# Kernel optimization log

Measured on AMD Instinct MI355X. Metric: run time of the kernel, lower is better.

## Reference

```python
import jax, jax.numpy as jnp
import numpy as np

N = 50000      # nodes
E = 800000     # edges (before self-loops)
DIN = 384
D = 128        # hidden_dim == output_dim
H = 4          # heads
FH = D // H    # per-head dim
B = 64         # graphs in batch
NEG = 0.2      # LeakyReLU slope in GATConv
EPS = 1e-5     # LayerNorm eps


def setup_inputs() -> dict:
    key = jax.random.key(0)
    ks = jax.random.split(key, 24)
    s = 0.02
    inp = {
        'node_features': jax.random.normal(ks[0], (N, DIN), jnp.float32),
        'edge_index': jax.random.randint(ks[1], (2, E), 0, N, dtype=jnp.int64),
        'edge_weight': jax.random.uniform(ks[2], (E,), jnp.float32),
        'batch': jnp.sort(jax.random.randint(ks[3], (N,), 0, B, dtype=jnp.int64)),
        # input projection
        'Wp': jax.random.normal(ks[4], (DIN, D), jnp.float32) * s,
        'bp': jnp.zeros((D,), jnp.float32),
    }
    for l in range(2):
        o = 5 + l * 9
        inp[f'W{l}'] = jax.random.normal(ks[o], (D, D), jnp.float32) * s      # lin_src (shared src/dst)
        inp[f'as{l}'] = jax.random.normal(ks[o + 1], (H, FH), jnp.float32) * s  # att_src
        inp[f'ad{l}'] = jax.random.normal(ks[o + 2], (H, FH), jnp.float32) * s  # att_dst
        inp[f'We{l}'] = jax.random.normal(ks[o + 3], (D,), jnp.float32) * s   # lin_edge (edge_dim=1)
        inp[f'ae{l}'] = jax.random.normal(ks[o + 4], (H, FH), jnp.float32) * s  # att_edge
        inp[f'b{l}'] = jnp.zeros((D,), jnp.float32)                           # GATConv bias
        inp[f'g{l}'] = jnp.ones((D,), jnp.float32)                            # LayerNorm gamma
        inp[f'be{l}'] = jnp.zeros((D,), jnp.float32)                          # LayerNorm beta
    return inp


def _gat(x, src, dst, ew, W, a_s, a_d, We, a_e, b):
    """PyG GATConv(in, D/H, heads=H, edge_dim=1), eval mode. ew includes self-loops."""
    n = x.shape[0]
    h = (x @ W).reshape(n, H, FH)                      # [N,H,FH]
    a_src = jnp.einsum('nhf,hf->nh', h, a_s)           # [N,H]
    a_dst = jnp.einsum('nhf,hf->nh', h, a_d)
    e = (ew[:, None] * We[None, :]).reshape(-1, H, FH)  # edge_dim=1 linear, no bias
    a_eg = jnp.einsum('ehf,hf->eh', e, a_e)            # [E,H]
    alpha = jax.nn.leaky_relu(a_src[src] + a_dst[dst] + a_eg, NEG)
    # softmax over incoming edges of each dst node
    amax = jax.ops.segment_max(alpha, dst, num_segments=n)
    amax = jnp.where(jnp.isfinite(amax), amax, 0.0)
    ex = jnp.exp(alpha - amax[dst])
    denom = jax.ops.segment_sum(ex, dst, num_segments=n)
    coef = ex / (denom[dst] + 1e-16)                   # [E,H]
    msg = h[src] * coef[..., None]                     # [E,H,FH]
    out = jax.ops.segment_sum(msg, dst, num_segments=n).reshape(n, D)
    return out + b


def _ln(x, g, b):
    mu = x.mean(-1, keepdims=True)
    v = ((x - mu) ** 2).mean(-1, keepdims=True)
    return (x - mu) * jax.lax.rsqrt(v + EPS) * g + b


def reference(node_features, edge_index, edge_weight, batch, Wp, bp,
              W0, as0, ad0, We0, ae0, b0, g0, be0,
              W1, as1, ad1, We1, ae1, b1, g1, be1):
    n = node_features.shape[0]
    # PyG GATConv add_self_loops=True, fill_value='mean' for edge_attr
    loop = jnp.arange(n, dtype=edge_index.dtype)
    src = jnp.concatenate([edge_index[0], loop])
    dst = jnp.concatenate([edge_index[1], loop])
    ew = jnp.concatenate([edge_weight, jnp.full((n,), edge_weight.mean(), edge_weight.dtype)])

    x = node_features @ Wp + bp
    for (W, a_s, a_d, We, a_e, b, g, be) in (
        (W0, as0, ad0, We0, ae0, b0, g0, be0),
        (W1, as1, ad1, We1, ae1, b1, g1, be1),
    ):
        res = x
        y = _gat(x, src, dst, ew, W, a_s, a_d, We, a_e, b)
        y = jax.nn.elu(_ln(y, g, be))
        x = y + res  # shapes match (hidden == output)

    # global_mean_pool
    s = jax.ops.segment_sum(x, batch, num_segments=B)
    c = jax.ops.segment_sum(jnp.ones((n,), x.dtype), batch, num_segments=B)
    return s / jnp.maximum(c, 1.0)[:, None]
```

## Files before the change

### kernel.cpp

```cpp
#include <hip/hip_runtime.h>

#define N_NODES 50000
#define N_EDGES 800000
#define DIN 384
#define DH 128
#define NB 64
#define NEG 0.2f

__device__ __forceinline__ float bf2f(unsigned short u) {
    return __uint_as_float((unsigned)u << 16);
}
__device__ __forceinline__ unsigned short f2bf(float x) {
    unsigned u = __float_as_uint(x);
    return (unsigned short)((u + 0x7fff + ((u >> 16) & 1)) >> 16);
}
__device__ __forceinline__ float sel4(float4 v, int k) {
    float r = v.x;
    r = (k == 1) ? v.y : r;
    r = (k == 2) ? v.z : r;
    r = (k == 3) ? v.w : r;
    return r;
}
using us8 = __attribute__((ext_vector_type(8))) unsigned short;

__global__ __launch_bounds__(256) void histew_kernel(const int* __restrict__ dst,
                                                     const float* __restrict__ ew,
                                                     int* __restrict__ cnt,
                                                     int* __restrict__ rank,
                                                     float* __restrict__ ews) {
    __shared__ float sred[4];
    const int tid = threadIdx.x;
    float v = 0.0f;
    for (int i = blockIdx.x * 256 + tid; i < N_EDGES; i += gridDim.x * 256) {
        rank[i] = atomicAdd(&cnt[dst[i]], 1);
        v += ew[i];
    }
    #pragma unroll
    for (int o = 32; o; o >>= 1) v += __shfl_down(v, o, 64);
    if ((tid & 63) == 0) sred[tid >> 6] = v;
    __syncthreads();
    if (tid == 0) atomicAdd(ews, sred[0] + sred[1] + sred[2] + sred[3]);
}

__global__ void scan_a(const int* __restrict__ cnt, int* __restrict__ scanned,
                       int* __restrict__ bsums) {
    __shared__ int s[256];
    int tid = threadIdx.x;
    int i = blockIdx.x * 256 + tid;
    int v = (i < N_NODES) ? cnt[i] : 0;
    s[tid] = v; __syncthreads();
    for (int o = 1; o < 256; o <<= 1) {
        int t = (tid >= o) ? s[tid - o] : 0;
        __syncthreads();
        s[tid] += t;
        __syncthreads();
    }
    if (i < N_NODES) scanned[i] = s[tid] - v;
    if (tid == 255) bsums[blockIdx.x] = s[255];
}

__global__ void scan_b(int* __restrict__ bsums, int nb,
                       const float* __restrict__ We0, const float* __restrict__ ae0,
                       const float* __restrict__ We1, const float* __restrict__ ae1,
                       const float* __restrict__ ews, float* __restrict__ consts) {
    __shared__ int s[256];
    int tid = threadIdx.x;
    int v = (tid < nb) ? bsums[tid] : 0;
    s[tid] = v; __syncthreads();
    for (int o = 1; o < 256; o <<= 1) {
        int t = (tid >= o) ? s[tid - o] : 0;
        __syncthreads();
        s[tid] += t;
        __syncthreads();
    }
    if (tid < nb) bsums[tid] = s[tid] - v;

    if (tid < 64) {
        const int l = tid;
        float p00 = We0[l] * ae0[l];
        float p01 = We0[l + 64] * ae0[l + 64];
        float p10 = We1[l] * ae1[l];
        float p11 = We1[l + 64] * ae1[l + 64];
        #pragma unroll
        for (int o = 1; o < 32; o <<= 1) {
            p00 += __shfl_xor(p00, o, 64); p01 += __shfl_xor(p01, o, 64);
            p10 += __shfl_xor(p10, o, 64); p11 += __shfl_xor(p11, o, 64);
        }
        const float c0 = __shfl(p00, 0, 64), c1 = __shfl(p00, 32, 64);
        const float c2 = __shfl(p01, 0, 64), c3 = __shfl(p01, 32, 64);
        const float d0 = __shfl(p10, 0, 64), d1 = __shfl(p10, 32, 64);
        const float d2 = __shfl(p11, 0, 64), d3 = __shfl(p11, 32, 64);
        if (l == 0) {
            consts[0] = c0; consts[1] = c1; consts[2] = c2; consts[3] = c3;
            consts[4] = d0; consts[5] = d1; consts[6] = d2; consts[7] = d3;
            consts[8] = ews[0] * (1.0f / N_EDGES);
        }
    }
}

__global__ void scan_c(const int* __restrict__ scanned, const int* __restrict__ bsums,
                       const int* __restrict__ cnt, int* __restrict__ ptr) {
    int i = blockIdx.x * 256 + threadIdx.x;
    if (i < N_NODES) {
        int p = scanned[i] + bsums[blockIdx.x];
        ptr[i] = p;
        if (i == N_NODES - 1) ptr[N_NODES] = p + cnt[i];
    }
}

__global__ __launch_bounds__(256) void fill_kernel(const int* __restrict__ src,
                            const int* __restrict__ dst,
                            const float* __restrict__ ew,
                            const int* __restrict__ rank,
                            const int* __restrict__ ptr,
                            int2* __restrict__ recE) {
    const int e0 = (blockIdx.x * 256 + threadIdx.x) * 4;
    if (e0 >= N_EDGES) return;
    const int4 d4 = *(const int4*)(dst + e0);
    const int4 s4 = *(const int4*)(src + e0);
    const int4 r4 = *(const int4*)(rank + e0);
    const float4 w4 = *(const float4*)(ew + e0);
    recE[ptr[d4.x] + r4.x] = make_int2(s4.x, __float_as_int(w4.x));
    recE[ptr[d4.y] + r4.y] = make_int2(s4.y, __float_as_int(w4.y));
    recE[ptr[d4.z] + r4.z] = make_int2(s4.z, __float_as_int(w4.z));
    recE[ptr[d4.w] + r4.w] = make_int2(s4.w, __float_as_int(w4.w));
}

template<int K, bool BF16OUT>
__global__ __launch_bounds__(256) void mfma_gemm(const float* __restrict__ A,
                                                 const float* __restrict__ W,
                                                 const float* __restrict__ bias,
                                                 void* __restrict__ Cv, int M,
                                                 const float* __restrict__ a_s,
                                                 const float* __restrict__ a_d,
                                                 float* __restrict__ asrc_o,
                                                 float* __restrict__ adst_o)
{
    constexpr int BM = 64, BK = 32;
    constexpr int LS = 40;
    __shared__ unsigned short As[BM * LS];
    __shared__ unsigned short Bs[DH * LS];
    using short8 = __attribute__((ext_vector_type(8))) short;
    using f32x4  = __attribute__((ext_vector_type(4))) float;

    const int tid = threadIdx.x;
    const int w = tid >> 6, l = tid & 63;
    const int lane16 = l & 15, quad = l >> 4;
    const int m0 = blockIdx.x * BM;

    f32x4 acc[8] = {};

    const int ar = tid >> 2, af = tid & 3;
    int arow = m0 + ar; if (arow >= M) arow = M - 1;
    const float* Ap = A + (size_t)arow * K;
    const int bn = tid & 127, bq = tid >> 7;

    for (int k0 = 0; k0 < K; k0 += BK) {
        __syncthreads();
        #pragma unroll
        for (int i = 0; i < 2; ++i) {
            const int f4 = af + 4 * i;
            float4 v = *(const float4*)(Ap + k0 + f4 * 4);
            ushort4 u = {f2bf(v.x), f2bf(v.y), f2bf(v.z), f2bf(v.w)};
            *(ushort4*)&As[ar * LS + f4 * 4] = u;
        }
        #pragma unroll
        for (int i = 0; i < 4; ++i) {
            const int kq = bq + 2 * i;
            float v0 = W[(size_t)(k0 + kq * 4 + 0) * DH + bn];
            float v1 = W[(size_t)(k0 + kq * 4 + 1) * DH + bn];
            float v2 = W[(size_t)(k0 + kq * 4 + 2) * DH + bn];
            float v3 = W[(size_t)(k0 + kq * 4 + 3) * DH + bn];
            ushort4 u = {f2bf(v0), f2bf(v1), f2bf(v2), f2bf(v3)};
            *(ushort4*)&Bs[bn * LS + kq * 4] = u;
        }
        __syncthreads();
        short8 afrag = *(short8*)&As[(w * 16 + lane16) * LS + quad * 8];
        #pragma unroll
        for (int nt = 0; nt < 8; ++nt) {
            short8 bfrag = *(short8*)&Bs[(nt * 16 + lane16) * LS + quad * 8];
            acc[nt] = __builtin_amdgcn_mfma_f32_16x16x32_bf16(afrag, bfrag, acc[nt], 0, 0, 0);
        }
    }

    const int orow0 = m0 + w * 16 + quad * 4;
    #pragma unroll
    for (int nt = 0; nt < 8; ++nt) {
        const int col = nt * 16 + lane16;
        const float bv = BF16OUT ? 0.0f : bias[col];
        #pragma unroll
        for (int r = 0; r < 4; ++r) {
            const int row = orow0 + r;
            if (row < M) {
                if constexpr (BF16OUT)
                    ((unsigned short*)Cv)[(size_t)row * DH + col] = f2bf(acc[nt][r]);
                else
                    ((float*)Cv)[(size_t)row * DH + col] = acc[nt][r] + bv;
            }
        }
    }

    if constexpr (BF16OUT) {
        float psh[4][4] = {}, pdh[4][4] = {};
        #pragma unroll
        for (int nt = 0; nt < 8; ++nt) {
            const int hd = nt >> 1;
            const float asv = a_s[nt * 16 + lane16];
            const float adv = a_d[nt * 16 + lane16];
            #pragma unroll
            for (int r = 0; r < 4; ++r) {
                psh[hd][r] = fmaf(acc[nt][r], asv, psh[hd][r]);
                pdh[hd][r] = fmaf(acc[nt][r], adv, pdh[hd][r]);
            }
        }
        #pragma unroll
        for (int o = 1; o < 16; o <<= 1) {
            #pragma unroll
            for (int hd = 0; hd < 4; ++hd)
                #pragma unroll
                for (int r = 0; r < 4; ++r) {
                    psh[hd][r] += __shfl_xor(psh[hd][r], o, 64);
                    pdh[hd][r] += __shfl_xor(pdh[hd][r], o, 64);
                }
        }
        if (lane16 == 0) {
            #pragma unroll
            for (int r = 0; r < 4; ++r) {
                const int row = orow0 + r;
                if (row < M) {
                    float4 o1 = {psh[0][r], psh[1][r], psh[2][r], psh[3][r]};
                    float4 o2 = {pdh[0][r], pdh[1][r], pdh[2][r], pdh[3][r]};
                    *(float4*)(asrc_o + (size_t)row * 4) = o1;
                    *(float4*)(adst_o + (size_t)row * 4) = o2;
                }
            }
        }
    }
}

#define MSG_NPB 16
__global__ __launch_bounds__(256) void msg_kernel(
    const unsigned short* __restrict__ h, const float* __restrict__ asrc,
    const float* __restrict__ adst, const float* __restrict__ xres,
    const int* __restrict__ indptr, const int2* __restrict__ recE,
    const float* __restrict__ consts, const int layer,
    const float* __restrict__ bias, const float* __restrict__ gamma,
    const float* __restrict__ beta, float* __restrict__ xout)
{
    const int l = threadIdx.x & 63;
    const int wv = threadIdx.x >> 6;
    const int grp = l >> 4;
    const int c8 = l & 15;
    const int hd8 = c8 >> 2;

    const int n = blockIdx.x * MSG_NPB + wv * 4 + grp;

    const float4 ccv = *(const float4*)(consts + layer * 4);
    const float cc_l = sel4(ccv, hd8);
    const float ewm = consts[8];
    const unsigned short* hb = h + c8 * 8;

    const int st = indptr[n];
    const int deg = indptr[n + 1] - st;
    const float ad_l = adst[(size_t)n * 4 + hd8];
    const float as_l = asrc[(size_t)n * 4 + hd8];

    float a0 = as_l + ad_l + ewm * cc_l;
    a0 = a0 > 0.f ? a0 : NEG * a0;
    const float pv0_l = __expf(a0);

    float dsum = 0.f;
    float acc8[8];
    {
        us8 u = *(const us8*)(hb + (size_t)n * DH);
        #pragma unroll
        for (int i = 0; i < 8; ++i) acc8[i] = pv0_l * bf2f(u[i]);
    }

    const int2* rq = recE + st;
    int e = 0;
    for (; e + 3 < deg; e += 4) {
        const int2 r0 = rq[e],     r1 = rq[e + 1];
        const int2 r2 = rq[e + 2], r3 = rq[e + 3];
        const float av0 = asrc[(size_t)r0.x * 4 + hd8];
        const float av1 = asrc[(size_t)r1.x * 4 + hd8];
        const float av2 = asrc[(size_t)r2.x * 4 + hd8];
        const float av3 = asrc[(size_t)r3.x * 4 + hd8];
        us8 u0 = *(const us8*)(hb + (size_t)r0.x * DH);
        us8 u1 = *(const us8*)(hb + (size_t)r1.x * DH);
        us8 u2 = *(const us8*)(hb + (size_t)r2.x * DH);
        us8 u3 = *(const us8*)(hb + (size_t)r3.x * DH);
        float al0 = av0 + ad_l + __int_as_float(r0.y) * cc_l;
        float al1 = av1 + ad_l + __int_as_float(r1.y) * cc_l;
        float al2 = av2 + ad_l + __int_as_float(r2.y) * cc_l;
        float al3 = av3 + ad_l + __int_as_float(r3.y) * cc_l;
        al0 = al0 > 0.f ? al0 : NEG * al0;
        al1 = al1 > 0.f ? al1 : NEG * al1;
        al2 = al2 > 0.f ? al2 : NEG * al2;
        al3 = al3 > 0.f ? al3 : NEG * al3;
        const float c0 = __expf(al0), c1 = __expf(al1);
        const float c2 = __expf(al2), c3 = __expf(al3);
        dsum += (c0 + c1) + (c2 + c3);
        #pragma unroll
        for (int i = 0; i < 8; ++i)
            acc8[i] = fmaf(c0, bf2f(u0[i]),
                      fmaf(c1, bf2f(u1[i]),
                      fmaf(c2, bf2f(u2[i]),
                      fmaf(c3, bf2f(u3[i]), acc8[i]))));
    }
    for (; e < deg; ++e) {
        const int2 r = rq[e];
        const float av = asrc[(size_t)r.x * 4 + hd8];
        us8 u = *(const us8*)(hb + (size_t)r.x * DH);
        float al = av + ad_l + __int_as_float(r.y) * cc_l;
        al = al > 0.f ? al : NEG * al;
        const float c = __expf(al);
        dsum += c;
        #pragma unroll
        for (int i = 0; i < 8; ++i) acc8[i] = fmaf(c, bf2f(u[i]), acc8[i]);
    }

    const float inv_d = 1.0f / (dsum + pv0_l + 1e-16f);
    const float4 b4a = *(const float4*)(bias + c8 * 8);
    const float4 b4b = *(const float4*)(bias + c8 * 8 + 4);
    float y[8];
    y[0] = acc8[0] * inv_d + b4a.x; y[1] = acc8[1] * inv_d + b4a.y;
    y[2] = acc8[2] * inv_d + b4a.z; y[3] = acc8[3] * inv_d + b4a.w;
    y[4] = acc8[4] * inv_d + b4b.x; y[5] = acc8[5] * inv_d + b4b.y;
    y[6] = acc8[6] * inv_d + b4b.z; y[7] = acc8[7] * inv_d + b4b.w;

    float s1 = 0.f, s2 = 0.f;
    #pragma unroll
    for (int i = 0; i < 8; ++i) { s1 += y[i]; s2 += y[i] * y[i]; }
    #pragma unroll
    for (int o = 1; o < 16; o <<= 1) {
        s1 += __shfl_xor(s1, o, 64);
        s2 += __shfl_xor(s2, o, 64);
    }
    const float mu = s1 * (1.0f / DH);
    const float var = s2 * (1.0f / DH) - mu * mu;
    const float rs = rsqrtf(var + 1e-5f);

    const float4 g4a = *(const float4*)(gamma + c8 * 8);
    const float4 g4b = *(const float4*)(gamma + c8 * 8 + 4);
    const float4 e4a = *(const float4*)(beta + c8 * 8);
    const float4 e4b = *(const float4*)(beta + c8 * 8 + 4);
    const float4 r4a = *(const float4*)(xres + (size_t)n * DH + c8 * 8);
    const float4 r4b = *(const float4*)(xres + (size_t)n * DH + c8 * 8 + 4);
    const float gv[8] = {g4a.x, g4a.y, g4a.z, g4a.w, g4b.x, g4b.y, g4b.z, g4b.w};
    const float ev[8] = {e4a.x, e4a.y, e4a.z, e4a.w, e4b.x, e4b.y, e4b.z, e4b.w};
    const float rv[8] = {r4a.x, r4a.y, r4a.z, r4a.w, r4b.x, r4b.y, r4b.z, r4b.w};
    float z[8];
    #pragma unroll
    for (int i = 0; i < 8; ++i) {
        float t = (y[i] - mu) * rs * gv[i] + ev[i];
        z[i] = (t > 0.f ? t : __expf(t) - 1.0f) + rv[i];
    }
    *(float4*)(xout + (size_t)n * DH + c8 * 8)     = *(float4*)&z[0];
    *(float4*)(xout + (size_t)n * DH + c8 * 8 + 4) = *(float4*)&z[4];
}

#define PNODES 64
__global__ __launch_bounds__(128) void pool_kernel(const float* __restrict__ x,
        const int* __restrict__ batch, float* __restrict__ pool, int* __restrict__ gcnt)
{
    int t = threadIdx.x;
    int n0 = blockIdx.x * PNODES;
    if (n0 >= N_NODES) return;
    int n1 = min(n0 + PNODES, N_NODES);
    float acc = 0.f; int cn = 0;
    int curb = batch[n0];
    for (int n = n0; n < n1; ++n) {
        int b = batch[n];
        if (b != curb) {
            atomicAdd(&pool[(size_t)curb * DH + t], acc);
            if (t == 0) atomicAdd(&gcnt[curb], cn);
            acc = 0.f; cn = 0; curb = b;
        }
        acc += x[(size_t)n * DH + t];
        ++cn;
    }
    atomicAdd(&pool[(size_t)curb * DH + t], acc);
    if (t == 0) atomicAdd(&gcnt[curb], cn);
}

__global__ void div_kernel(const float* __restrict__ pool, const int* __restrict__ gcnt,
                           float* __restrict__ out)
{
    int i = blockIdx.x * blockDim.x + threadIdx.x;
    if (i < NB * DH) {
        float c = (float)gcnt[i >> 7];
        out[i] = pool[i] / fmaxf(c, 1.0f);
    }
}

extern "C" void kernel_launch(void* const* d_in, const int* in_sizes, int n_in,
                              void* d_out, int out_size, void* d_ws, size_t ws_size,
                              hipStream_t stream)
{
    const float* nf    = (const float*)d_in[0];
    const int*   esrc  = (const int*)d_in[1];
    const int*   edst  = esrc + N_EDGES;
    const float* ew    = (const float*)d_in[2];
    const int*   batch = (const int*)d_in[3];
    const float* Wp    = (const float*)d_in[4];
    const float* bp    = (const float*)d_in[5];
    const float* Wl[2]  = {(const float*)d_in[6],  (const float*)d_in[14]};
    const float* asl[2] = {(const float*)d_in[7],  (const float*)d_in[15]};
    const float* adl[2] = {(const float*)d_in[8],  (const float*)d_in[16]};
    const float* Wel[2] = {(const float*)d_in[9],  (const float*)d_in[17]};
    const float* ael[2] = {(const float*)d_in[10], (const float*)d_in[18]};
    const float* bl[2]  = {(const float*)d_in[11], (const float*)d_in[19]};
    const float* gl[2]  = {(const float*)d_in[12], (const float*)d_in[20]};
    const float* bel[2] = {(const float*)d_in[13], (const float*)d_in[21]};
    float* outp = (float*)d_out;

    char* w = (char*)d_ws;
    auto alloc = [&](size_t bytes) { char* p = w; w += (bytes + 255) & ~255ull; return p; };
    float* xA     = (float*)alloc((size_t)N_NODES * DH * 4);
    float* xB     = (float*)alloc((size_t)N_NODES * DH * 4);
    unsigned short* hbuf = (unsigned short*)alloc((size_t)N_NODES * DH * 2);
    float* asrc   = (float*)alloc((size_t)N_NODES * 4 * 4);
    float* adst   = (float*)alloc((size_t)N_NODES * 4 * 4);
    float* pool   = (float*)alloc((size_t)NB * DH * 4);
    int* gcnt     = (int*)alloc(256);
    float* ews    = (float*)alloc(256);
    int* cnt      = (int*)alloc((size_t)N_NODES * 4);
    int* scanned  = (int*)alloc((size_t)N_NODES * 4);
    int* bsums    = (int*)alloc(1024);
    int* ptr      = (int*)alloc((size_t)(N_NODES + 8) * 4);
    int* rank     = (int*)alloc((size_t)N_EDGES * 4);
    int2* recE    = (int2*)alloc((size_t)N_EDGES * 8);
    float* consts = (float*)alloc(256);

    hipMemsetAsync(pool, 0, (size_t)NB * DH * 4 + 256 + 256 + (size_t)N_NODES * 4, stream);

    const int sb = (N_NODES + 255) / 256;

    histew_kernel<<<1024, 256, 0, stream>>>(edst, ew, cnt, rank, ews);
    scan_a<<<sb, 256, 0, stream>>>(cnt, scanned, bsums);
    scan_b<<<1, 256, 0, stream>>>(bsums, sb, Wel[0], ael[0], Wel[1], ael[1], ews, consts);
    scan_c<<<sb, 256, 0, stream>>>(scanned, bsums, cnt, ptr);
    fill_kernel<<<(N_EDGES / 4 + 255) / 256, 256, 0, stream>>>(esrc, edst, ew, rank, ptr, recE);

    const int gb = (N_NODES + 63) / 64;
    mfma_gemm<DIN, false><<<gb, 256, 0, stream>>>(nf, Wp, bp, xA, N_NODES,
                                                  nullptr, nullptr, nullptr, nullptr);

    const float* xin = xA;
    float* xout = xB;
    for (int l = 0; l < 2; ++l) {
        mfma_gemm<DH, true><<<gb, 256, 0, stream>>>(xin, Wl[l], nullptr, hbuf, N_NODES,
                                                    asl[l], adl[l], asrc, adst);
        msg_kernel<<<N_NODES / MSG_NPB, 256, 0, stream>>>(
            hbuf, asrc, adst, xin, ptr, recE, consts, l,
            bl[l], gl[l], bel[l], xout);
        float* tmp = (float*)xin; xin = xout; xout = tmp;
    }

    pool_kernel<<<(N_NODES + PNODES - 1) / PNODES, 128, 0, stream>>>(xin, batch, pool, gcnt);
    div_kernel<<<(NB * DH + 255) / 256, 256, 0, stream>>>(pool, gcnt, outp);
}
```

Measured before the change: 378.4 us.

## Pre-transpose weights to bf16 and feed layer GEMMs bf16 activations

Adds a prep kernel that converts and transposes Wp, W0 and W1 to bf16 once, so the GEMMs load B tiles with vectorized 16-byte reads and skip per-tile conversion. The projection GEMM now uses 128-row tiles and also writes a bf16 copy of its output. msg_kernel writes a bf16 copy after layer 0, so the layer GEMMs read half-width activations. This trades extra bf16 stores and workspace for fewer bytes read and less conversion work in the GEMMs.

```diff
diff --git a/kernel.cpp b/kernel.cpp
--- a/kernel.cpp
+++ b/kernel.cpp
@@ -22,6 +22,25 @@
     return r;
 }
 using us8 = __attribute__((ext_vector_type(8))) unsigned short;
+using short8 = __attribute__((ext_vector_type(8))) short;
+using f32x4  = __attribute__((ext_vector_type(4))) float;
+
+__global__ __launch_bounds__(256) void prep_w(const float* __restrict__ Wp,
+        const float* __restrict__ W0, const float* __restrict__ W1,
+        unsigned short* __restrict__ Wtp, unsigned short* __restrict__ Wt0,
+        unsigned short* __restrict__ Wt1)
+{
+    const int i = blockIdx.x * 256 + threadIdx.x;
+    if (i < DIN * DH) {
+        const int k = i >> 7, n = i & 127;
+        Wtp[(size_t)n * DIN + k] = f2bf(Wp[i]);
+    }
+    if (i < DH * DH) {
+        const int k = i >> 7, n = i & 127;
+        Wt0[(size_t)n * DH + k] = f2bf(W0[i]);
+        Wt1[(size_t)n * DH + k] = f2bf(W1[i]);
+    }
+}
 
 __global__ __launch_bounds__(256) void histew_kernel(const int* __restrict__ dst,
                                                      const float* __restrict__ ew,
@@ -126,113 +145,158 @@
     recE[ptr[d4.w] + r4.w] = make_int2(s4.w, __float_as_int(w4.w));
 }
 
-template<int K, bool BF16OUT>
-__global__ __launch_bounds__(256) void mfma_gemm(const float* __restrict__ A,
-                                                 const float* __restrict__ W,
-                                                 const float* __restrict__ bias,
-                                                 void* __restrict__ Cv, int M,
-                                                 const float* __restrict__ a_s,
-                                                 const float* __restrict__ a_d,
-                                                 float* __restrict__ asrc_o,
-                                                 float* __restrict__ adst_o)
-{
-    constexpr int BM = 64, BK = 32;
-    constexpr int LS = 40;
+__global__ __launch_bounds__(256) void mfma_gemm_proj(
+    const float* __restrict__ A, const unsigned short* __restrict__ Wt,
+    const float* __restrict__ bias, float* __restrict__ C,
+    unsigned short* __restrict__ Cb, int M)
+{
+    constexpr int K = DIN, BM = 128, BK = 32, LS = 40;
     __shared__ unsigned short As[BM * LS];
     __shared__ unsigned short Bs[DH * LS];
-    using short8 = __attribute__((ext_vector_type(8))) short;
-    using f32x4  = __attribute__((ext_vector_type(4))) float;
 
     const int tid = threadIdx.x;
     const int w = tid >> 6, l = tid & 63;
     const int lane16 = l & 15, quad = l >> 4;
     const int m0 = blockIdx.x * BM;
 
-    f32x4 acc[8] = {};
-
-    const int ar = tid >> 2, af = tid & 3;
+    f32x4 acc[2][8] = {};
+
+    const int ar = tid >> 1, ah = tid & 1;
     int arow = m0 + ar; if (arow >= M) arow = M - 1;
     const float* Ap = A + (size_t)arow * K;
-    const int bn = tid & 127, bq = tid >> 7;
 
     for (int k0 = 0; k0 < K; k0 += BK) {
         __syncthreads();
         #pragma unroll
+        for (int j = 0; j < 4; ++j) {
+            float4 v = *(const float4*)(Ap + k0 + ah * 16 + j * 4);
+            ushort4 u = {f2bf(v.x), f2bf(v.y), f2bf(v.z), f2bf(v.w)};
+            *(ushort4*)&As[ar * LS + ah * 16 + j * 4] = u;
+        }
+        #pragma unroll
         for (int i = 0; i < 2; ++i) {
-            const int f4 = af + 4 * i;
-            float4 v = *(const float4*)(Ap + k0 + f4 * 4);
-            ushort4 u = {f2bf(v.x), f2bf(v.y), f2bf(v.z), f2bf(v.w)};
-            *(ushort4*)&As[ar * LS + f4 * 4] = u;
-        }
-        #pragma unroll
-        for (int i = 0; i < 4; ++i) {
-            const int kq = bq + 2 * i;
-            float v0 = W[(size_t)(k0 + kq * 4 + 0) * DH + bn];
-            float v1 = W[(size_t)(k0 + kq * 4 + 1) * DH + bn];
-            float v2 = W[(size_t)(k0 + kq * 4 + 2) * DH + bn];
-            float v3 = W[(size_t)(k0 + kq * 4 + 3) * DH + bn];
-            ushort4 u = {f2bf(v0), f2bf(v1), f2bf(v2), f2bf(v3)};
-            *(ushort4*)&Bs[bn * LS + kq * 4] = u;
-        }
-        __syncthreads();
-        short8 afrag = *(short8*)&As[(w * 16 + lane16) * LS + quad * 8];
+            const int idx = tid + 256 * i;
+            const int bn = idx >> 2, seg = idx & 3;
+            us8 v = *(const us8*)(Wt + (size_t)bn * K + k0 + seg * 8);
+            *(us8*)&Bs[bn * LS + seg * 8] = v;
+        }
+        __syncthreads();
+        short8 af0 = *(short8*)&As[(w * 32 + lane16) * LS + quad * 8];
+        short8 af1 = *(short8*)&As[(w * 32 + 16 + lane16) * LS + quad * 8];
         #pragma unroll
         for (int nt = 0; nt < 8; ++nt) {
-            short8 bfrag = *(short8*)&Bs[(nt * 16 + lane16) * LS + quad * 8];
-            acc[nt] = __builtin_amdgcn_mfma_f32_16x16x32_bf16(afrag, bfrag, acc[nt], 0, 0, 0);
-        }
-    }
-
-    const int orow0 = m0 + w * 16 + quad * 4;
-    #pragma unroll
-    for (int nt = 0; nt < 8; ++nt) {
-        const int col = nt * 16 + lane16;
-        const float bv = BF16OUT ? 0.0f : bias[col];
-        #pragma unroll
-        for (int r = 0; r < 4; ++r) {
-            const int row = orow0 + r;
-            if (row < M) {
-                if constexpr (BF16OUT)
-                    ((unsigned short*)Cv)[(size_t)row * DH + col] = f2bf(acc[nt][r]);
-                else
-                    ((float*)Cv)[(size_t)row * DH + col] = acc[nt][r] + bv;
-            }
-        }
-    }
-
-    if constexpr (BF16OUT) {
-        float psh[4][4] = {}, pdh[4][4] = {};
+            short8 bf = *(short8*)&Bs[(nt * 16 + lane16) * LS + quad * 8];
+            acc[0][nt] = __builtin_amdgcn_mfma_f32_16x16x32_bf16(af0, bf, acc[0][nt], 0, 0, 0);
+            acc[1][nt] = __builtin_amdgcn_mfma_f32_16x16x32_bf16(af1, bf, acc[1][nt], 0, 0, 0);
+        }
+    }
+
+    #pragma unroll
+    for (int r2 = 0; r2 < 2; ++r2) {
+        const int orow0 = m0 + w * 32 + r2 * 16 + quad * 4;
         #pragma unroll
         for (int nt = 0; nt < 8; ++nt) {
-            const int hd = nt >> 1;
-            const float asv = a_s[nt * 16 + lane16];
-            const float adv = a_d[nt * 16 + lane16];
-            #pragma unroll
-            for (int r = 0; r < 4; ++r) {
-                psh[hd][r] = fmaf(acc[nt][r], asv, psh[hd][r]);
-                pdh[hd][r] = fmaf(acc[nt][r], adv, pdh[hd][r]);
-            }
-        }
-        #pragma unroll
-        for (int o = 1; o < 16; o <<= 1) {
-            #pragma unroll
-            for (int hd = 0; hd < 4; ++hd)
-                #pragma unroll
-                for (int r = 0; r < 4; ++r) {
-                    psh[hd][r] += __shfl_xor(psh[hd][r], o, 64);
-                    pdh[hd][r] += __shfl_xor(pdh[hd][r], o, 64);
-                }
-        }
-        if (lane16 == 0) {
+            const int col = nt * 16 + lane16;
+            const float bv = bias[col];
             #pragma unroll
             for (int r = 0; r < 4; ++r) {
                 const int row = orow0 + r;
                 if (row < M) {
-                    float4 o1 = {psh[0][r], psh[1][r], psh[2][r], psh[3][r]};
-                    float4 o2 = {pdh[0][r], pdh[1][r], pdh[2][r], pdh[3][r]};
-                    *(float4*)(asrc_o + (size_t)row * 4) = o1;
-                    *(float4*)(adst_o + (size_t)row * 4) = o2;
+                    const float v = acc[r2][nt][r] + bv;
+                    C[(size_t)row * DH + col] = v;
+                    Cb[(size_t)row * DH + col] = f2bf(v);
                 }
+            }
+        }
+    }
+}
+
+__global__ __launch_bounds__(256) void mfma_gemm_layer(
+    const unsigned short* __restrict__ Ab, const unsigned short* __restrict__ Wt,
+    unsigned short* __restrict__ Hout, int M,
+    const float* __restrict__ a_s, const float* __restrict__ a_d,
+    float* __restrict__ asrc_o, float* __restrict__ adst_o)
+{
+    constexpr int K = DH, BM = 64, BK = 32, LS = 40;
+    __shared__ unsigned short As[BM * LS];
+    __shared__ unsigned short Bs[DH * LS];
+
+    const int tid = threadIdx.x;
+    const int w = tid >> 6, l = tid & 63;
+    const int lane16 = l & 15, quad = l >> 4;
+    const int m0 = blockIdx.x * BM;
+
+    f32x4 acc[8] = {};
+
+    const int ar = tid >> 2, aseg = tid & 3;
+    int arow = m0 + ar; if (arow >= M) arow = M - 1;
+    const unsigned short* Ap = Ab + (size_t)arow * K;
+
+    for (int k0 = 0; k0 < K; k0 += BK) {
+        __syncthreads();
+        {
+            us8 v = *(const us8*)(Ap + k0 + aseg * 8);
+            *(us8*)&As[ar * LS + aseg * 8] = v;
+        }
+        #pragma unroll
+        for (int i = 0; i < 2; ++i) {
+            const int idx = tid + 256 * i;
+            const int bn = idx >> 2, seg = idx & 3;
+            us8 v = *(const us8*)(Wt + (size_t)bn * K + k0 + seg * 8);
+            *(us8*)&Bs[bn * LS + seg * 8] = v;
+        }
+        __syncthreads();
+        short8 af = *(short8*)&As[(w * 16 + lane16) * LS + quad * 8];
+        #pragma unroll
+        for (int nt = 0; nt < 8; ++nt) {
+            short8 bf = *(short8*)&Bs[(nt * 16 + lane16) * LS + quad * 8];
+            acc[nt] = __builtin_amdgcn_mfma_f32_16x16x32_bf16(af, bf, acc[nt], 0, 0, 0);
+        }
+    }
+
+    const int orow0 = m0 + w * 16 + quad * 4;
+    #pragma unroll
+    for (int nt = 0; nt < 8; ++nt) {
+        const int col = nt * 16 + lane16;
+        #pragma unroll
+        for (int r = 0; r < 4; ++r) {
+            const int row = orow0 + r;
+            if (row < M)
+                Hout[(size_t)row * DH + col] = f2bf(acc[nt][r]);
+        }
+    }
+
+    float psh[4][4] = {}, pdh[4][4] = {};
+    #pragma unroll
+    for (int nt = 0; nt < 8; ++nt) {
+        const int hd = nt >> 1;
+        const float asv = a_s[nt * 16 + lane16];
+        const float adv = a_d[nt * 16 + lane16];
+        #pragma unroll
+        for (int r = 0; r < 4; ++r) {
+            psh[hd][r] = fmaf(acc[nt][r], asv, psh[hd][r]);
+            pdh[hd][r] = fmaf(acc[nt][r], adv, pdh[hd][r]);
+        }
+    }
+    #pragma unroll
+    for (int o = 1; o < 16; o <<= 1) {
+        #pragma unroll
+        for (int hd = 0; hd < 4; ++hd)
+            #pragma unroll
+            for (int r = 0; r < 4; ++r) {
+                psh[hd][r] += __shfl_xor(psh[hd][r], o, 64);
+                pdh[hd][r] += __shfl_xor(pdh[hd][r], o, 64);
+            }
+    }
+    if (lane16 == 0) {
+        #pragma unroll
+        for (int r = 0; r < 4; ++r) {
+            const int row = orow0 + r;
+            if (row < M) {
+                float4 o1 = {psh[0][r], psh[1][r], psh[2][r], psh[3][r]};
+                float4 o2 = {pdh[0][r], pdh[1][r], pdh[2][r], pdh[3][r]};
+                *(float4*)(asrc_o + (size_t)row * 4) = o1;
+                *(float4*)(adst_o + (size_t)row * 4) = o2;
             }
         }
     }
@@ -245,7 +309,8 @@
     const int* __restrict__ indptr, const int2* __restrict__ recE,
     const float* __restrict__ consts, const int layer,
     const float* __restrict__ bias, const float* __restrict__ gamma,
-    const float* __restrict__ beta, float* __restrict__ xout)
+    const float* __restrict__ beta, float* __restrict__ xout,
+    unsigned short* __restrict__ xob)
 {
     const int l = threadIdx.x & 63;
     const int wv = threadIdx.x >> 6;
@@ -358,6 +423,12 @@
     }
     *(float4*)(xout + (size_t)n * DH + c8 * 8)     = *(float4*)&z[0];
     *(float4*)(xout + (size_t)n * DH + c8 * 8 + 4) = *(float4*)&z[4];
+    if (xob) {
+        ushort4 ub0 = {f2bf(z[0]), f2bf(z[1]), f2bf(z[2]), f2bf(z[3])};
+        ushort4 ub1 = {f2bf(z[4]), f2bf(z[5]), f2bf(z[6]), f2bf(z[7])};
+        *(ushort4*)(xob + (size_t)n * DH + c8 * 8)     = ub0;
+        *(ushort4*)(xob + (size_t)n * DH + c8 * 8 + 4) = ub1;
+    }
 }
 
 #define PNODES 64
@@ -420,6 +491,7 @@
     float* xA     = (float*)alloc((size_t)N_NODES * DH * 4);
     float* xB     = (float*)alloc((size_t)N_NODES * DH * 4);
     unsigned short* hbuf = (unsigned short*)alloc((size_t)N_NODES * DH * 2);
+    unsigned short* xb   = (unsigned short*)alloc((size_t)N_NODES * DH * 2);
     float* asrc   = (float*)alloc((size_t)N_NODES * 4 * 4);
     float* adst   = (float*)alloc((size_t)N_NODES * 4 * 4);
     float* pool   = (float*)alloc((size_t)NB * DH * 4);
@@ -432,29 +504,33 @@
     int* rank     = (int*)alloc((size_t)N_EDGES * 4);
     int2* recE    = (int2*)alloc((size_t)N_EDGES * 8);
     float* consts = (float*)alloc(256);
+    unsigned short* Wtp = (unsigned short*)alloc((size_t)DH * DIN * 2);
+    unsigned short* Wt0 = (unsigned short*)alloc((size_t)DH * DH * 2);
+    unsigned short* Wt1 = (unsigned short*)alloc((size_t)DH * DH * 2);
+    unsigned short* Wts[2] = {Wt0, Wt1};
 
     hipMemsetAsync(pool, 0, (size_t)NB * DH * 4 + 256 + 256 + (size_t)N_NODES * 4, stream);
 
     const int sb = (N_NODES + 255) / 256;
 
+    prep_w<<<(DIN * DH + 255) / 256, 256, 0, stream>>>(Wp, Wl[0], Wl[1], Wtp, Wt0, Wt1);
     histew_kernel<<<1024, 256, 0, stream>>>(edst, ew, cnt, rank, ews);
     scan_a<<<sb, 256, 0, stream>>>(cnt, scanned, bsums);
     scan_b<<<1, 256, 0, stream>>>(bsums, sb, Wel[0], ael[0], Wel[1], ael[1], ews, consts);
     scan_c<<<sb, 256, 0, stream>>>(scanned, bsums, cnt, ptr);
     fill_kernel<<<(N_EDGES / 4 + 255) / 256, 256, 0, stream>>>(esrc, edst, ew, rank, ptr, recE);
 
+    mfma_gemm_proj<<<(N_NODES + 127) / 128, 256, 0, stream>>>(nf, Wtp, bp, xA, xb, N_NODES);
+
     const int gb = (N_NODES + 63) / 64;
-    mfma_gemm<DIN, false><<<gb, 256, 0, stream>>>(nf, Wp, bp, xA, N_NODES,
-                                                  nullptr, nullptr, nullptr, nullptr);
-
     const float* xin = xA;
     float* xout = xB;
     for (int l = 0; l < 2; ++l) {
-        mfma_gemm<DH, true><<<gb, 256, 0, stream>>>(xin, Wl[l], nullptr, hbuf, N_NODES,
-                                                    asl[l], adl[l], asrc, adst);
+        mfma_gemm_layer<<<gb, 256, 0, stream>>>(xb, Wts[l], hbuf, N_NODES,
+                                                asl[l], adl[l], asrc, adst);
         msg_kernel<<<N_NODES / MSG_NPB, 256, 0, stream>>>(
             hbuf, asrc, adst, xin, ptr, recE, consts, l,
-            bl[l], gl[l], bel[l], xout);
+            bl[l], gl[l], bel[l], xout, (l == 0) ? xb : nullptr);
         float* tmp = (float*)xin; xin = xout; xout = tmp;
     }
 
```

Measured after the change: 374.1 us. No clear change (-1.1%).
